# Kernel optimization log

Hardware: AMD Instinct MI355X
Metric: run time of the kernel (lower is better)

The kernel has to match this reference:

```python
import jax, jax.numpy as jnp
import numpy as np

EPS = 1e-10  # PyTorch Adagrad epsilon convention: denom = sqrt(m) + eps


def setup_inputs() -> dict:
    key = jax.random.key(0)
    k1, k2, k3, k4 = jax.random.split(key, 4)
    N, V, D = 262144, 500000, 64
    return {
        "gradients": jax.random.normal(k1, (N, D), dtype=jnp.float32),
        "weights": jax.random.normal(k2, (V, D), dtype=jnp.float32),
        "moments": jax.random.uniform(k3, (V, D), dtype=jnp.float32),
        "indices": jax.random.randint(k4, (N,), 0, V, dtype=jnp.int64),
        "learning_rate": jnp.ones((), dtype=jnp.float32),
        "valid_count": 200000,  # python int (static)
    }


def reference(gradients, weights, moments, indices, learning_rate, valid_count):
    # Sparse Adagrad: gather rows by index, m += g^2, w -= lr*g/(sqrt(m)+eps), scatter back.
    N = gradients.shape[0]
    valid = (jnp.arange(N) < valid_count)[:, None]          # [N,1] mask of valid rows
    g = jnp.where(valid, gradients, jnp.zeros((), gradients.dtype))  # [N,D]

    # Accumulate squared grads into moments (duplicate indices accumulate).
    moments_new = moments.at[indices].add(g * g)            # [V,D]

    # Per-row denominator uses the fully-accumulated moment of that index.
    denom = jnp.sqrt(moments_new[indices]) + EPS            # [N,D] gather
    weights_new = weights.at[indices].add(-learning_rate * g / denom)  # [V,D]

    return weights_new, moments_new
```

## Files before the change

### kernel.cpp

```cpp
#include <hip/hip_runtime.h>

#define ADAGRAD_EPS 1e-10f

__global__ void copy_init_kernel(const float4* __restrict__ w4,
                                 const float4* __restrict__ m4,
                                 float4* __restrict__ ow4,
                                 float4* __restrict__ om4,
                                 long long n4) {
    long long i = (long long)blockIdx.x * blockDim.x + threadIdx.x;
    long long stride = (long long)gridDim.x * blockDim.x;
    for (; i < n4; i += stride) {
        ow4[i] = w4[i];
        om4[i] = m4[i];
    }
}

__global__ void scatter_m_kernel(const float* __restrict__ g,
                                 const int* __restrict__ idx,
                                 const int* __restrict__ valid_count,
                                 float* __restrict__ out_m) {
    int vc = *valid_count;
    int t = blockIdx.x * blockDim.x + threadIdx.x;
    int row = t >> 6;
    if (row >= vc) return;
    float gv = g[t];
    int i = idx[row];
    atomicAdd(&out_m[(long long)i * 64 + (t & 63)], gv * gv);
}

__global__ void update_w_kernel(const float* __restrict__ g,
                                const int* __restrict__ idx,
                                const int* __restrict__ valid_count,
                                const float* __restrict__ lr_p,
                                const float* __restrict__ out_m,
                                float* __restrict__ out_w) {
    int vc = *valid_count;
    int t = blockIdx.x * blockDim.x + threadIdx.x;
    int row = t >> 6;
    if (row >= vc) return;
    int d = t & 63;
    float gv = g[t];
    int i = idx[row];
    long long off = (long long)i * 64 + d;
    float m = out_m[off];
    float lr = *lr_p;
    float upd = -lr * gv / (sqrtf(m) + ADAGRAD_EPS);
    atomicAdd(&out_w[off], upd);
}

extern "C" void kernel_launch(void* const* d_in, const int* in_sizes, int n_in,
                              void* d_out, int out_size, void* d_ws, size_t ws_size,
                              hipStream_t stream) {
    const float* g  = (const float*)d_in[0];
    const float* w  = (const float*)d_in[1];
    const float* m  = (const float*)d_in[2];
    const int*   idx = (const int*)d_in[3];
    const float* lr  = (const float*)d_in[4];
    const int*   vc  = (const int*)d_in[5];

    long long ND = in_sizes[0];
    long long VD = in_sizes[1];

    float* out_w = (float*)d_out;
    float* out_m = (float*)d_out + VD;

    long long n4 = VD / 4;
    copy_init_kernel<<<4096, 256, 0, stream>>>(
        (const float4*)w, (const float4*)m, (float4*)out_w, (float4*)out_m, n4);

    int blocks = (int)((ND + 255) / 256);
    scatter_m_kernel<<<blocks, 256, 0, stream>>>(g, idx, vc, out_m);
    update_w_kernel<<<blocks, 256, 0, stream>>>(g, idx, vc, lr, out_m, out_w);
}
```

Measured before the change: 548.8 us.

## Replace atomic scatter with per-row linked lists and fused owner-computes apply

Builds per-vocabulary-row linked lists of gradient rows with atomicExch, then one kernel per output row walks its list, sums g and g^2, and writes both the new moment and the new weight. The full-table copy, the float atomics on the moments and the second atomic pass on the weights are folded into a single streaming pass over weights and moments. Because the denominator is shared by every duplicate of a row, summing g before dividing is mathematically equivalent, though the floating-point summation order differs. The list walks are dependent pointer-chasing loads with divergent lengths, and the head/next arrays need workspace.

Result: faster. 467.9 us (-14.7%).

```diff
diff --git a/kernel.cpp b/kernel.cpp
--- a/kernel.cpp
+++ b/kernel.cpp
@@ -2,73 +2,99 @@
 
 #define ADAGRAD_EPS 1e-10f
 
-__global__ void copy_init_kernel(const float4* __restrict__ w4,
-                                 const float4* __restrict__ m4,
-                                 float4* __restrict__ ow4,
-                                 float4* __restrict__ om4,
-                                 long long n4) {
-    long long i = (long long)blockIdx.x * blockDim.x + threadIdx.x;
-    long long stride = (long long)gridDim.x * blockDim.x;
-    for (; i < n4; i += stride) {
-        ow4[i] = w4[i];
-        om4[i] = m4[i];
-    }
+
+__global__ void init_head_kernel(int* __restrict__ head, int V) {
+    int i = blockIdx.x * blockDim.x + threadIdx.x;
+    if (i < V) head[i] = -1;
 }
 
-__global__ void scatter_m_kernel(const float* __restrict__ g,
-                                 const int* __restrict__ idx,
-                                 const int* __restrict__ valid_count,
-                                 float* __restrict__ out_m) {
-    int vc = *valid_count;
-    int t = blockIdx.x * blockDim.x + threadIdx.x;
-    int row = t >> 6;
-    if (row >= vc) return;
-    float gv = g[t];
-    int i = idx[row];
-    atomicAdd(&out_m[(long long)i * 64 + (t & 63)], gv * gv);
+__global__ void build_lists_kernel(const int* __restrict__ idx,
+                                   const int* __restrict__ vc_p,
+                                   int* __restrict__ head,
+                                   int* __restrict__ next) {
+    int vc = *vc_p;
+    int r = blockIdx.x * blockDim.x + threadIdx.x;
+    if (r >= vc) return;
+    int i = idx[r];
+    next[r] = atomicExch(&head[i], r);
 }
 
-__global__ void update_w_kernel(const float* __restrict__ g,
-                                const int* __restrict__ idx,
-                                const int* __restrict__ valid_count,
-                                const float* __restrict__ lr_p,
-                                const float* __restrict__ out_m,
-                                float* __restrict__ out_w) {
-    int vc = *valid_count;
+__global__ void apply_kernel(const float4* __restrict__ g4,
+                             const float4* __restrict__ w4,
+                             const float4* __restrict__ m4,
+                             const int* __restrict__ head,
+                             const int* __restrict__ next,
+                             const float* __restrict__ lr_p,
+                             float4* __restrict__ ow4,
+                             float4* __restrict__ om4,
+                             int V) {
     int t = blockIdx.x * blockDim.x + threadIdx.x;
-    int row = t >> 6;
-    if (row >= vc) return;
-    int d = t & 63;
-    float gv = g[t];
-    int i = idx[row];
-    long long off = (long long)i * 64 + d;
-    float m = out_m[off];
+    int v = t >> 4;
+    if (v >= V) return;
+    int d = t & 15;
+    long long off = (long long)v * 16 + d;
+
+    float4 wv = w4[off];
+    float4 mv = m4[off];
+    int r = head[v];
+
+    if (r < 0) {
+        ow4[off] = wv;
+        om4[off] = mv;
+        return;
+    }
+
+    float4 s1 = make_float4(0.f, 0.f, 0.f, 0.f);
+    float4 s2 = make_float4(0.f, 0.f, 0.f, 0.f);
+    while (r >= 0) {
+        float4 gv = g4[(long long)r * 16 + d];
+        s1.x += gv.x; s1.y += gv.y; s1.z += gv.z; s1.w += gv.w;
+        s2.x += gv.x * gv.x; s2.y += gv.y * gv.y;
+        s2.z += gv.z * gv.z; s2.w += gv.w * gv.w;
+        r = next[r];
+    }
+
+    float4 mn;
+    mn.x = mv.x + s2.x; mn.y = mv.y + s2.y;
+    mn.z = mv.z + s2.z; mn.w = mv.w + s2.w;
+    om4[off] = mn;
+
     float lr = *lr_p;
-    float upd = -lr * gv / (sqrtf(m) + ADAGRAD_EPS);
-    atomicAdd(&out_w[off], upd);
+    float4 wn;
+    wn.x = wv.x - lr * s1.x / (sqrtf(mn.x) + ADAGRAD_EPS);
+    wn.y = wv.y - lr * s1.y / (sqrtf(mn.y) + ADAGRAD_EPS);
+    wn.z = wv.z - lr * s1.z / (sqrtf(mn.z) + ADAGRAD_EPS);
+    wn.w = wv.w - lr * s1.w / (sqrtf(mn.w) + ADAGRAD_EPS);
+    ow4[off] = wn;
 }
 
 extern "C" void kernel_launch(void* const* d_in, const int* in_sizes, int n_in,
                               void* d_out, int out_size, void* d_ws, size_t ws_size,
                               hipStream_t stream) {
-    const float* g  = (const float*)d_in[0];
-    const float* w  = (const float*)d_in[1];
-    const float* m  = (const float*)d_in[2];
+    const float* g   = (const float*)d_in[0];
+    const float* w   = (const float*)d_in[1];
+    const float* m   = (const float*)d_in[2];
     const int*   idx = (const int*)d_in[3];
     const float* lr  = (const float*)d_in[4];
     const int*   vc  = (const int*)d_in[5];
 
     long long ND = in_sizes[0];
     long long VD = in_sizes[1];
+    int N = (int)(ND / 64);
+    int V = (int)(VD / 64);
 
     float* out_w = (float*)d_out;
     float* out_m = (float*)d_out + VD;
 
-    long long n4 = VD / 4;
-    copy_init_kernel<<<4096, 256, 0, stream>>>(
-        (const float4*)w, (const float4*)m, (float4*)out_w, (float4*)out_m, n4);
+    int* head = (int*)d_ws;
+    int* next = head + V;
 
-    int blocks = (int)((ND + 255) / 256);
-    scatter_m_kernel<<<blocks, 256, 0, stream>>>(g, idx, vc, out_m);
-    update_w_kernel<<<blocks, 256, 0, stream>>>(g, idx, vc, lr, out_m, out_w);
+    init_head_kernel<<<(V + 255) / 256, 256, 0, stream>>>(head, V);
+
+    build_lists_kernel<<<(N + 255) / 256, 256, 0, stream>>>(idx, vc, head, next);
+
+    long long apply_threads = (long long)V * 16;
+    apply_kernel<<<(int)((apply_threads + 255) / 256), 256, 0, stream>>>(
+        (const float4*)g, (const float4*)w, (const float4*)m,
+        head, next, lr, (float4*)out_w, (float4*)out_m, V);
 }
```
